# Kernel optimization log

Measured on AMD Instinct MI355X. Metric: run time of the kernel, lower is better.

Reference implementation:

```python
import jax, jax.numpy as jnp
import numpy as np

L, D, H, FF, V = 8, 768, 8, 2048, 32000
MAXLEN, TMAX = 512, 4
S = MAXLEN * TMAX  # 2048 context length
HD = D // H
EPS = 1e-4  # layer_norm_eps from module defaults


def setup_inputs() -> dict:
    key = jax.random.key(0)
    ks = jax.random.split(key, 16)
    s = 0.02
    B = 1
    rn = lambda k, shape: jax.random.normal(k, shape, jnp.float32) * s
    # sinusoidal positional encoding over MAXLEN real-token positions
    pos = np.arange(MAXLEN)[:, None]
    div = np.exp(np.arange(0, D, 2) * (-np.log(10000.0) / D))
    pe = np.zeros((MAXLEN, D), np.float32)
    pe[:, 0::2] = np.sin(pos * div)
    pe[:, 1::2] = np.cos(pos * div)
    return {
        "state_embeddings": jax.random.normal(ks[0], (B, S, D), jnp.float32),
        "padding_mask": jnp.zeros((B, S), bool),
        "pe": jnp.asarray(pe),
        "thought_emb": rn(ks[1], (TMAX, D)),
        "w_qkv": rn(ks[2], (L, 3 * D, D)),
        "b_qkv": jnp.zeros((L, 3 * D), jnp.float32),
        "w_out": rn(ks[3], (L, D, D)),
        "b_out": jnp.zeros((L, D), jnp.float32),
        "ln1_g": jnp.ones((L, D), jnp.float32),
        "ln1_b": jnp.zeros((L, D), jnp.float32),
        "ln2_g": jnp.ones((L, D), jnp.float32),
        "ln2_b": jnp.zeros((L, D), jnp.float32),
        "w_ff1": rn(ks[4], (L, FF, D)),
        "b_ff1": jnp.zeros((L, FF), jnp.float32),
        "w_ff2": rn(ks[5], (L, D, FF)),
        "b_ff2": jnp.zeros((L, D), jnp.float32),
        "fn_g": jnp.ones((D,), jnp.float32),
        "fn_b": jnp.zeros((D,), jnp.float32),
        "w_policy": rn(ks[6], (V, D)),
        "w_v1": rn(ks[7], (FF, D)),
        "b_v1": jnp.zeros((FF,), jnp.float32),
        "w_v2": rn(ks[8], (1, FF)),
        "b_v2": jnp.zeros((1,), jnp.float32),
        "n_thoughts_taken": 3,
    }


def _layer_norm(x, g, b):
    m = x.mean(-1, keepdims=True)
    v = ((x - m) ** 2).mean(-1, keepdims=True)
    return (x - m) / jnp.sqrt(v + EPS) * g + b


def reference(state_embeddings, padding_mask, pe, thought_emb, w_qkv, b_qkv, w_out, b_out, ln1_g, ln1_b, ln2_g, ln2_b, w_ff1, b_ff1, w_ff2, b_ff2, fn_g, fn_b, w_policy, w_v1, b_v1, w_v2, b_v2, n_thoughts_taken):
    tt = int(n_thoughts_taken)
    T = tt + 1  # block size (token + thoughts taken)
    B = state_embeddings.shape[0]
    R = MAXLEN  # real_token_count: all token slots real (no padding)
    # --- DualPositionalEncoding ---
    x = state_embeddings[:, :MAXLEN * T].reshape(B, MAXLEN, T, D)
    x = x + pe[None, :, None, :] + thought_emb[None, None, :T, :]
    x = x.reshape(B, MAXLEN * T, D)
    x = jnp.pad(x, ((0, 0), (0, S - MAXLEN * T), (0, 0)))
    # --- ThoughtsFormer block-causal mask (keep=True means attend) ---
    i = jnp.arange(S)
    tok, off = i // T, i % T
    same_block = (tok[:, None] == tok[None, :]) & (off[:, None] >= off[None, :]) & (tok[:, None] < R)
    global_cols = (off[None, :] == 0) & (tok[None, :] < R) & (i[:, None] > i[None, :]) & (i[:, None] < R * T)
    keep = (same_block | global_cols)[None, None] & (~padding_mask)[:, None, None, :]
    scale = 1.0 / np.sqrt(HD)

    def layer(h, p):
        wq, bq, wo, bo, g1, b1, g2, b2, wf1, bf1, wf2, bf2 = p
        # pre-norm self-attention
        y = _layer_norm(h, g1, b1)
        q, k, v = jnp.split(y @ wq.T + bq, 3, axis=-1)
        q = q.reshape(B, S, H, HD)
        k = k.reshape(B, S, H, HD)
        v = v.reshape(B, S, H, HD)
        scores = jnp.einsum('bihd,bjhd->bhij', q, k) * scale
        attn = jax.nn.softmax(jnp.where(keep, scores, -jnp.inf), axis=-1)
        o = jnp.einsum('bhij,bjhd->bihd', attn, v).reshape(B, S, D)
        h = h + o @ wo.T + bo
        # pre-norm FFN with exact (erf) GELU
        y = _layer_norm(h, g2, b2)
        h = h + jax.nn.gelu(y @ wf1.T + bf1, approximate=False) @ wf2.T + bf2
        h = jnp.where(jnp.isnan(h), 0.0, h)
        return h, None

    x, _ = jax.lax.scan(layer, x, (w_qkv, b_qkv, w_out, b_out, ln1_g, ln1_b, ln2_g, ln2_b, w_ff1, b_ff1, w_ff2, b_ff2))
    x = _layer_norm(x, fn_g, fn_b)  # TransformerEncoder final norm
    logits = x @ w_policy.T  # policy head (no bias)
    values = jax.nn.gelu(x @ w_v1.T + b_v1, approximate=False) @ w_v2.T + b_v2
    return logits, values
```

## Files before the change

kernel.cpp:

```cpp
#include <hip/hip_runtime.h>
#include <math.h>

#define S_TOT 2048
#define DMODEL 768
#define QKVD 2304
#define NHEAD 8
#define HDIM 96
#define FFDIM 2048
#define VOCAB 32000
#define MAXLEN_C 512
#define POL_CHUNK 3200
#define VLT_LD 2080
#define NEG_BIG (-3.0e38f)
#define M_INIT (-1.0e30f)
#define QK_SCALE 0.10206207261596575f

typedef __bf16 bf16x8 __attribute__((ext_vector_type(8)));
typedef float f32x4 __attribute__((ext_vector_type(4)));
typedef unsigned short u16x8 __attribute__((ext_vector_type(8)));
typedef unsigned short u16x4 __attribute__((ext_vector_type(4)));

__device__ __forceinline__ float gelu_exact(float x) {
  return 0.5f * x * (1.0f + erff(x * 0.70710678118654752f));
}

__device__ __forceinline__ float bf2f(unsigned short u) {
  union { unsigned int i; float f; } v;
  v.i = ((unsigned int)u) << 16;
  return v.f;
}

__device__ __forceinline__ unsigned short f2bf(float f) {
  union { float f; unsigned int i; } v;
  v.f = f;
  unsigned int x = v.i;
  return (unsigned short)((x + 0x7fffu + ((x >> 16) & 1u)) >> 16);
}

__device__ __forceinline__ unsigned int pack2bf(float a, float b) {
  return (unsigned int)f2bf(a) | ((unsigned int)f2bf(b) << 16);
}

__device__ __forceinline__ void gload_lds16(const unsigned short* g, unsigned short* l) {
  __builtin_amdgcn_global_load_lds(
      (const __attribute__((address_space(1))) unsigned int*)g,
      (__attribute__((address_space(3))) unsigned int*)l, 16, 0, 0);
}

__global__ __launch_bounds__(256) void embed_kernel(
    const float* __restrict__ se, const float* __restrict__ pe,
    const float* __restrict__ th, const int* __restrict__ ntt,
    float* __restrict__ X) {
  int idx = blockIdx.x * 256 + threadIdx.x;
  if (idx >= S_TOT * DMODEL) return;
  int p = idx / DMODEL;
  int d = idx - p * DMODEL;
  int T = ntt[0] + 1;
  float v = 0.0f;
  if (p < MAXLEN_C * T) {
    v = se[idx] + pe[(p / T) * DMODEL + d] + th[(p % T) * DMODEL + d];
  }
  X[idx] = v;
}

__global__ __launch_bounds__(256) void ln_bf_kernel(
    const float* __restrict__ X, const float* __restrict__ g,
    const float* __restrict__ b, unsigned short* __restrict__ Y) {
  __shared__ float red[4];
  const int row = blockIdx.x;
  const int tid = threadIdx.x;
  const float* x = X + (size_t)row * DMODEL;
  float v0 = x[tid], v1 = x[tid + 256], v2 = x[tid + 512];
  float s = v0 + v1 + v2;
  for (int o = 32; o; o >>= 1) s += __shfl_xor(s, o);
  if ((tid & 63) == 0) red[tid >> 6] = s;
  __syncthreads();
  float mean = (red[0] + red[1] + red[2] + red[3]) * (1.0f / DMODEL);
  float d0 = v0 - mean, d1 = v1 - mean, d2 = v2 - mean;
  float s2 = d0 * d0 + d1 * d1 + d2 * d2;
  for (int o = 32; o; o >>= 1) s2 += __shfl_xor(s2, o);
  __syncthreads();
  if ((tid & 63) == 0) red[tid >> 6] = s2;
  __syncthreads();
  float var = (red[0] + red[1] + red[2] + red[3]) * (1.0f / DMODEL);
  float rstd = rsqrtf(var + 1e-4f);
  unsigned short* y = Y + (size_t)row * DMODEL;
  y[tid]       = f2bf(d0 * rstd * g[tid]       + b[tid]);
  y[tid + 256] = f2bf(d1 * rstd * g[tid + 256] + b[tid + 256]);
  y[tid + 512] = f2bf(d2 * rstd * g[tid + 512] + b[tid + 512]);
}

__global__ __launch_bounds__(256) void cvt_kernel(
    const float* __restrict__ s, unsigned short* __restrict__ d, int n) {
  int i = (blockIdx.x * 256 + threadIdx.x) * 4;
  if (i >= n) return;
  float4 v = *(const float4*)(s + i);
  u16x4 o;
  o[0] = f2bf(v.x); o[1] = f2bf(v.y); o[2] = f2bf(v.z); o[3] = f2bf(v.w);
  *(u16x4*)(d + i) = o;
}

__global__ __launch_bounds__(256) void cvt4_kernel(
    const float* __restrict__ s0, const float* __restrict__ s1,
    const float* __restrict__ s2, const float* __restrict__ s3,
    unsigned short* __restrict__ d0, unsigned short* __restrict__ d1,
    unsigned short* __restrict__ d2, unsigned short* __restrict__ d3,
    int n0, int n1, int n2, int n3) {
  int i = (blockIdx.x * 256 + threadIdx.x) * 4;
  const float* s;
  unsigned short* d;
  if (i < n0) { s = s0; d = d0; }
  else if (i < n0 + n1) { i -= n0; s = s1; d = d1; }
  else if (i < n0 + n1 + n2) { i -= n0 + n1; s = s2; d = d2; }
  else if (i < n0 + n1 + n2 + n3) { i -= n0 + n1 + n2; s = s3; d = d3; }
  else return;
  float4 v = *(const float4*)(s + i);
  u16x4 o;
  o[0] = f2bf(v.x); o[1] = f2bf(v.y); o[2] = f2bf(v.z); o[3] = f2bf(v.w);
  *(u16x4*)(d + i) = o;
}

__global__ __launch_bounds__(256) void cvt6_kernel(
    const float* __restrict__ s0, const float* __restrict__ s1,
    const float* __restrict__ s2, const float* __restrict__ s3,
    const float* __restrict__ s4, const float* __restrict__ s5,
    unsigned short* __restrict__ d0, unsigned short* __restrict__ d1,
    unsigned short* __restrict__ d2, unsigned short* __restrict__ d3,
    unsigned short* __restrict__ d4, unsigned short* __restrict__ d5,
    int n0, int n1, int n2, int n3, int n4, int n5) {
  int i = (blockIdx.x * 256 + threadIdx.x) * 4;
  const float* s;
  unsigned short* d;
  if (i < n0) { s = s0; d = d0; }
  else if (i < n0 + n1) { i -= n0; s = s1; d = d1; }
  else if (i < n0 + n1 + n2) { i -= n0 + n1; s = s2; d = d2; }
  else if (i < n0 + n1 + n2 + n3) { i -= n0 + n1 + n2; s = s3; d = d3; }
  else if (i < n0 + n1 + n2 + n3 + n4) { i -= n0 + n1 + n2 + n3; s = s4; d = d4; }
  else if (i < n0 + n1 + n2 + n3 + n4 + n5) { i -= n0 + n1 + n2 + n3 + n4; s = s5; d = d5; }
  else return;
  float4 v = *(const float4*)(s + i);
  u16x4 o;
  o[0] = f2bf(v.x); o[1] = f2bf(v.y); o[2] = f2bf(v.z); o[3] = f2bf(v.w);
  *(u16x4*)(d + i) = o;
}

__global__ __launch_bounds__(256) void gemm_bf16_kernel(
    const unsigned short* __restrict__ A, const unsigned short* __restrict__ B,
    const float* __restrict__ bias, const float* __restrict__ res,
    void* __restrict__ Cout, int M, int N, int K, int ldc, int act, int outbf,
    int swiz) {
  __shared__ __align__(16) unsigned short As[128 * 32];
  __shared__ __align__(16) unsigned short Bs[128 * 32];
  const int t = threadIdx.x;
  const int w = t >> 6, l = t & 63;
  int n_blk, m_blk;
  if (swiz) {
    const int g = blockIdx.x;
    const int chunk = gridDim.x >> 3;
    const int logical = (g & 7) * chunk + (g >> 3);
    m_blk = logical & 15;
    n_blk = logical >> 4;
  } else {
    n_blk = blockIdx.x; m_blk = blockIdx.y;
  }
  const int n0 = n_blk * 128, i0 = m_blk * 128;
  const int wr = w >> 1, wc = w & 1;
  const int lr = l & 15;
  const int koff = (l >> 4) * 8;

  f32x4 acc[4][4] = {};

  const int srow = t >> 2;
  const int scol = (t & 3) * 8;
  const unsigned short* Ag = A + (size_t)(i0 + srow) * K + scol;
  const unsigned short* Bg = B + (size_t)(n0 + srow) * K + scol;
  unsigned short* Alds0 = &As[(w << 9)];
  unsigned short* Alds1 = &As[2048 + (w << 9)];
  unsigned short* Blds0 = &Bs[(w << 9)];
  unsigned short* Blds1 = &Bs[2048 + (w << 9)];

  for (int k0 = 0; k0 < K; k0 += 32) {
    __syncthreads();
    gload_lds16(Ag + k0, Alds0);
    gload_lds16(Ag + (size_t)64 * K + k0, Alds1);
    gload_lds16(Bg + k0, Blds0);
    gload_lds16(Bg + (size_t)64 * K + k0, Blds1);
    __syncthreads();

    bf16x8 af[4], bfr[4];
#pragma unroll
    for (int fi = 0; fi < 4; ++fi)
      af[fi] = *(const bf16x8*)&As[(wr * 64 + fi * 16 + lr) * 32 + koff];
#pragma unroll
    for (int fj = 0; fj < 4; ++fj)
      bfr[fj] = *(const bf16x8*)&Bs[(wc * 64 + fj * 16 + lr) * 32 + koff];
#pragma unroll
    for (int fi = 0; fi < 4; ++fi)
#pragma unroll
      for (int fj = 0; fj < 4; ++fj)
        acc[fi][fj] = __builtin_amdgcn_mfma_f32_16x16x32_bf16(
            bfr[fj], af[fi], acc[fi][fj], 0, 0, 0);
  }

  const int mloc = l & 15, ng = (l >> 4) * 4;
#pragma unroll
  for (int fi = 0; fi < 4; ++fi) {
    const int i = i0 + wr * 64 + fi * 16 + mloc;
    const size_t rowbase = (size_t)i * ldc;
#pragma unroll
    for (int fj = 0; fj < 4; ++fj) {
      const int nb = n0 + wc * 64 + fj * 16 + ng;
      float z0 = acc[fi][fj][0], z1 = acc[fi][fj][1];
      float z2 = acc[fi][fj][2], z3 = acc[fi][fj][3];
      if (bias) {
        float4 bv = *(const float4*)(bias + nb);
        z0 += bv.x; z1 += bv.y; z2 += bv.z; z3 += bv.w;
      }
      if (act) {
        z0 = gelu_exact(z0); z1 = gelu_exact(z1);
        z2 = gelu_exact(z2); z3 = gelu_exact(z3);
      }
      if (res) {
        float4 rv = *(const float4*)(res + rowbase + nb);
        z0 += rv.x; z1 += rv.y; z2 += rv.z; z3 += rv.w;
      }
      if (outbf) {
        u16x4 o;
        o[0] = f2bf(z0); o[1] = f2bf(z1); o[2] = f2bf(z2); o[3] = f2bf(z3);
        *(u16x4*)((unsigned short*)Cout + rowbase + nb) = o;
      } else {
        *(float4*)((float*)Cout + rowbase + nb) = make_float4(z0, z1, z2, z3);
      }
    }
  }
}

__global__ __launch_bounds__(256) void gemm64_bf16_kernel(
    const unsigned short* __restrict__ A, const unsigned short* __restrict__ B,
    const float* __restrict__ bias, const float* __restrict__ res,
    void* __restrict__ Cout, int M, int N, int K, int ldc, int act, int outbf) {
  __shared__ __align__(16) unsigned short As[2 * 64 * 32];
  __shared__ __align__(16) unsigned short Bs[2 * 64 * 32];
  const int t = threadIdx.x;
  const int w = t >> 6, l = t & 63;
  const int n0 = blockIdx.x * 64, i0 = blockIdx.y * 64;
  const int wr = w >> 1, wc = w & 1;
  const int lr = l & 15;
  const int koff = (l >> 4) * 8;

  f32x4 acc[2][2] = {};

  const int srow = t >> 2;
  const int scol = (t & 3) * 8;
  const unsigned short* Ag = A + (size_t)(i0 + srow) * K + scol;
  const unsigned short* Bg = B + (size_t)(n0 + srow) * K + scol;
  unsigned short* Alds0 = &As[(w << 9)];
  unsigned short* Alds1 = &As[2048 + (w << 9)];
  unsigned short* Blds0 = &Bs[(w << 9)];
  unsigned short* Blds1 = &Bs[2048 + (w << 9)];

  for (int k0 = 0; k0 < K; k0 += 64) {
    __syncthreads();
    gload_lds16(Ag + k0, Alds0);
    gload_lds16(Ag + k0 + 32, Alds1);
    gload_lds16(Bg + k0, Blds0);
    gload_lds16(Bg + k0 + 32, Blds1);
    __syncthreads();

    bf16x8 af[2][2], bfr[2][2];
#pragma unroll
    for (int fi = 0; fi < 2; ++fi)
#pragma unroll
      for (int kk = 0; kk < 2; ++kk)
        af[fi][kk] = *(const bf16x8*)&As[kk * 2048 + (wr * 32 + fi * 16 + lr) * 32 + koff];
#pragma unroll
    for (int fj = 0; fj < 2; ++fj)
#pragma unroll
      for (int kk = 0; kk < 2; ++kk)
        bfr[fj][kk] = *(const bf16x8*)&Bs[kk * 2048 + (wc * 32 + fj * 16 + lr) * 32 + koff];
#pragma unroll
    for (int fi = 0; fi < 2; ++fi)
#pragma unroll
      for (int fj = 0; fj < 2; ++fj)
#pragma unroll
        for (int kk = 0; kk < 2; ++kk)
          acc[fi][fj] = __builtin_amdgcn_mfma_f32_16x16x32_bf16(
              bfr[fj][kk], af[fi][kk], acc[fi][fj], 0, 0, 0);
  }

  const int mloc = l & 15, ng = (l >> 4) * 4;
#pragma unroll
  for (int fi = 0; fi < 2; ++fi) {
    const int i = i0 + wr * 32 + fi * 16 + mloc;
    const size_t rowbase = (size_t)i * ldc;
#pragma unroll
    for (int fj = 0; fj < 2; ++fj) {
      const int nb = n0 + wc * 32 + fj * 16 + ng;
      float z0 = acc[fi][fj][0], z1 = acc[fi][fj][1];
      float z2 = acc[fi][fj][2], z3 = acc[fi][fj][3];
      if (bias) {
        float4 bv = *(const float4*)(bias + nb);
        z0 += bv.x; z1 += bv.y; z2 += bv.z; z3 += bv.w;
      }
      if (act) {
        z0 = gelu_exact(z0); z1 = gelu_exact(z1);
        z2 = gelu_exact(z2); z3 = gelu_exact(z3);
      }
      if (res) {
        float4 rv = *(const float4*)(res + rowbase + nb);
        z0 += rv.x; z1 += rv.y; z2 += rv.z; z3 += rv.w;
      }
      if (outbf) {
        u16x4 o;
        o[0] = f2bf(z0); o[1] = f2bf(z1); o[2] = f2bf(z2); o[3] = f2bf(z3);
        *(u16x4*)((unsigned short*)Cout + rowbase + nb) = o;
      } else {
        *(float4*)((float*)Cout + rowbase + nb) = make_float4(z0, z1, z2, z3);
      }
    }
  }
}

__global__ __launch_bounds__(256) void repack_kernel(
    const unsigned short* __restrict__ qkv, const int* __restrict__ ntt,
    unsigned short* __restrict__ Kg, unsigned short* __restrict__ Vgt,
    unsigned short* __restrict__ Vlt) {
  __shared__ unsigned short vt[64][104];
  const int pb = blockIdx.x * 64, h = blockIdx.y;
  const int T = ntt[0] + 1;
  const int tid = threadIdx.x;

  for (int idx = tid; idx < 64 * 96; idx += 256) {
    int pp = idx / 96, d = idx - pp * 96;
    vt[pp][d] = qkv[(size_t)(pb + pp) * QKVD + 2 * DMODEL + h * HDIM + d];
  }
  const int firstpp = (T - pb % T) % T;
  const int ng = (64 - firstpp + T - 1) / T;
  for (int idx = tid; idx < ng * 96; idx += 256) {
    int gi = idx / 96, d = idx - gi * 96;
    int p = pb + firstpp + gi * T;
    int g = p / T;
    if (g < MAXLEN_C)
      Kg[((size_t)h * 512 + g) * 96 + d] = qkv[(size_t)p * QKVD + DMODEL + h * HDIM + d];
  }
  __syncthreads();
  for (int idx = tid; idx < 96 * 64; idx += 256) {
    int d = idx >> 6, pp = idx & 63;
    Vlt[((size_t)h * 96 + d) * VLT_LD + pb + pp] = vt[pp][d];
  }
  for (int idx = tid; idx < ng * 96; idx += 256) {
    int d = idx / ng, gi = idx - d * ng;
    int pp = firstpp + gi * T;
    int g = (pb + pp) / T;
    if (g < MAXLEN_C && d < 96)
      Vgt[((size_t)h * 96 + d) * 512 + g] = vt[pp][d];
  }
}

__global__ __launch_bounds__(256) void attn_flash_kernel(
    const unsigned short* __restrict__ qkv, const unsigned short* __restrict__ Kg,
    const unsigned short* __restrict__ Vgt, const unsigned short* __restrict__ Vlt,
    const int* __restrict__ ntt, unsigned short* __restrict__ att) {
  __shared__ float Osh[4][96][17];
  __shared__ float Msh[4][16];
  __shared__ float Lsh[4][16];
  const int s = blockIdx.x, h = blockIdx.y;
  const int T = ntt[0] + 1;
  const int tid = threadIdx.x;
  const int w = tid >> 6, l = tid & 63;
  const int q15 = l & 15, grp = l >> 4;
  const int p0 = s * 16;
  const int p = p0 + q15;
  const int myTok = p / T;

  const unsigned short* qrow = qkv + (size_t)p * QKVD + h * HDIM + grp * 8;
  bf16x8 qf0 = *(const bf16x8*)(qrow);
  bf16x8 qf1 = *(const bf16x8*)(qrow + 32);
  bf16x8 qf2 = *(const bf16x8*)(qrow + 64);

  float m_run = M_INIT, l_run = 0.0f;
  f32x4 oacc[6] = {};

  const int gmax = (p0 + 15) / T;
  const int KP = (gmax >> 5) + 1;
  const unsigned short* KgH = Kg + (size_t)h * 512 * 96;
  const unsigned short* VgH = Vgt + (size_t)h * 96 * 512;

  for (int kp = w; kp < KP; kp += 4) {
    f32x4 s0 = {}, s1 = {};
    const unsigned short* k0r = KgH + (size_t)(kp * 32 + q15) * 96 + grp * 8;
    const unsigned short* k1r = k0r + 16 * 96;
    {
      bf16x8 a0 = *(const bf16x8*)(k0r);
      bf16x8 a1 = *(const bf16x8*)(k1r);
      bf16x8 b0 = *(const bf16x8*)(k0r + 32);
      bf16x8 b1 = *(const bf16x8*)(k1r + 32);
      bf16x8 c0 = *(const bf16x8*)(k0r + 64);
      bf16x8 c1 = *(const bf16x8*)(k1r + 64);
      __builtin_amdgcn_s_setprio(1);
      s0 = __builtin_amdgcn_mfma_f32_16x16x32_bf16(a0, qf0, s0, 0, 0, 0);
      s1 = __builtin_amdgcn_mfma_f32_16x16x32_bf16(a1, qf0, s1, 0, 0, 0);
      s0 = __builtin_amdgcn_mfma_f32_16x16x32_bf16(b0, qf1, s0, 0, 0, 0);
      s1 = __builtin_amdgcn_mfma_f32_16x16x32_bf16(b1, qf1, s1, 0, 0, 0);
      s0 = __builtin_amdgcn_mfma_f32_16x16x32_bf16(c0, qf2, s0, 0, 0, 0);
      s1 = __builtin_amdgcn_mfma_f32_16x16x32_bf16(c1, qf2, s1, 0, 0, 0);
      __builtin_amdgcn_s_setprio(0);
    }
    float sc[8];
#pragma unroll
    for (int e = 0; e < 4; ++e) {
      int g = kp * 32 + grp * 4 + e;
      sc[e] = (g * T <= p) ? s0[e] * QK_SCALE : NEG_BIG;
      g += 16;
      sc[4 + e] = (g * T <= p) ? s1[e] * QK_SCALE : NEG_BIG;
    }
    float tmax = sc[0];
#pragma unroll
    for (int e = 1; e < 8; ++e) tmax = fmaxf(tmax, sc[e]);
    tmax = fmaxf(tmax, __shfl_xor(tmax, 16));
    tmax = fmaxf(tmax, __shfl_xor(tmax, 32));
    float mnew = fmaxf(m_run, tmax);
    float alpha = __expf(m_run - mnew);
    float pv[8], ps = 0.0f;
#pragma unroll
    for (int e = 0; e < 8; ++e) { pv[e] = __expf(sc[e] - mnew); ps += pv[e]; }
    ps += __shfl_xor(ps, 16);
    ps += __shfl_xor(ps, 32);
    l_run = l_run * alpha + ps;
    m_run = mnew;
#pragma unroll
    for (int dt = 0; dt < 6; ++dt) oacc[dt] *= alpha;
    unsigned int pk0[2], pk1[2];
    pk0[0] = pack2bf(pv[0], pv[1]); pk0[1] = pack2bf(pv[2], pv[3]);
    pk1[0] = pack2bf(pv[4], pv[5]); pk1[1] = pack2bf(pv[6], pv[7]);
    union { unsigned int u[4]; bf16x8 v; } pf;
#pragma unroll
    for (int w2 = 0; w2 < 4; ++w2) {
      int src = (((grp & 1) << 1) + (w2 >> 1)) * 16 + q15;
      int y0 = __shfl((int)pk0[w2 & 1], src);
      int y1 = __shfl((int)pk1[w2 & 1], src);
      pf.u[w2] = (grp >> 1) ? (unsigned int)y1 : (unsigned int)y0;
    }
    __builtin_amdgcn_s_setprio(1);
#pragma unroll
    for (int dt = 0; dt < 6; ++dt) {
      bf16x8 vf = *(const bf16x8*)(VgH + (size_t)(dt * 16 + q15) * 512 + kp * 32 + grp * 8);
      oacc[dt] = __builtin_amdgcn_mfma_f32_16x16x32_bf16(vf, pf.v, oacc[dt], 0, 0, 0);
    }
    __builtin_amdgcn_s_setprio(0);
  }

  if (w == 3) {
    f32x4 s0 = {};
    const unsigned short* kl = qkv + (size_t)(p0 + q15) * QKVD + DMODEL + h * HDIM + grp * 8;
    __builtin_amdgcn_s_setprio(1);
    s0 = __builtin_amdgcn_mfma_f32_16x16x32_bf16(*(const bf16x8*)(kl), qf0, s0, 0, 0, 0);
    s0 = __builtin_amdgcn_mfma_f32_16x16x32_bf16(*(const bf16x8*)(kl + 32), qf1, s0, 0, 0, 0);
    s0 = __builtin_amdgcn_mfma_f32_16x16x32_bf16(*(const bf16x8*)(kl + 64), qf2, s0, 0, 0, 0);
    __builtin_amdgcn_s_setprio(0);
    float sc[4];
#pragma unroll
    for (int e = 0; e < 4; ++e) {
      int pk = p0 + grp * 4 + e;
      bool ok = (pk / T == myTok) && (pk % T != 0) && (pk <= p);
      sc[e] = ok ? s0[e] * QK_SCALE : NEG_BIG;
    }
    float tmax = fmaxf(fmaxf(sc[0], sc[1]), fmaxf(sc[2], sc[3]));
    tmax = fmaxf(tmax, __shfl_xor(tmax, 16));
    tmax = fmaxf(tmax, __shfl_xor(tmax, 32));
    float mnew = fmaxf(m_run, tmax);
    float alpha = __expf(m_run - mnew);
    float pv[4], ps = 0.0f;
#pragma unroll
    for (int e = 0; e < 4; ++e) { pv[e] = __expf(sc[e] - mnew); ps += pv[e]; }
    ps += __shfl_xor(ps, 16);
    ps += __shfl_xor(ps, 32);
    l_run = l_run * alpha + ps;
    m_run = mnew;
#pragma unroll
    for (int dt = 0; dt < 6; ++dt) oacc[dt] *= alpha;
    unsigned int pk0[2];
    pk0[0] = pack2bf(pv[0], pv[1]); pk0[1] = pack2bf(pv[2], pv[3]);
    union { unsigned int u[4]; bf16x8 v; } pf;
#pragma unroll
    for (int w2 = 0; w2 < 4; ++w2) {
      int src = (((grp & 1) << 1) + (w2 >> 1)) * 16 + q15;
      int y0 = __shfl((int)pk0[w2 & 1], src);
      pf.u[w2] = (grp >> 1) ? 0u : (unsigned int)y0;
    }
    __builtin_amdgcn_s_setprio(1);
#pragma unroll
    for (int dt = 0; dt < 6; ++dt) {
      bf16x8 vf = *(const bf16x8*)(Vlt + ((size_t)h * 96 + dt * 16 + q15) * VLT_LD + p0 + grp * 8);
      oacc[dt] = __builtin_amdgcn_mfma_f32_16x16x32_bf16(vf, pf.v, oacc[dt], 0, 0, 0);
    }
    __builtin_amdgcn_s_setprio(0);
  }

  if (l < 16) { Msh[w][l] = m_run; Lsh[w][l] = l_run; }
#pragma unroll
  for (int dt = 0; dt < 6; ++dt)
#pragma unroll
    for (int e = 0; e < 4; ++e)
      Osh[w][dt * 16 + grp * 4 + e][q15] = oacc[dt][e];
  __syncthreads();

  {
    const int q = tid & 15, dg = tid >> 4;
    float m0 = Msh[0][q], m1 = Msh[1][q], m2 = Msh[2][q], m3 = Msh[3][q];
    float ms = fmaxf(fmaxf(m0, m1), fmaxf(m2, m3));
    float c0 = __expf(m0 - ms), c1 = __expf(m1 - ms);
    float c2 = __expf(m2 - ms), c3 = __expf(m3 - ms);
    float lsum = c0 * Lsh[0][q] + c1 * Lsh[1][q] + c2 * Lsh[2][q] + c3 * Lsh[3][q];
    float rinv = 1.0f / lsum;
    unsigned short* orow = att + (size_t)(p0 + q) * DMODEL + h * HDIM;
#pragma unroll
    for (int j = 0; j < 6; ++j) {
      int d = dg * 6 + j;
      float o = c0 * Osh[0][d][q] + c1 * Osh[1][d][q] +
                c2 * Osh[2][d][q] + c3 * Osh[3][d][q];
      orow[d] = f2bf(o * rinv);
    }
  }
}

__global__ __launch_bounds__(256) void v2_kernel(
    const unsigned short* __restrict__ F1, const float* __restrict__ w2,
    const float* __restrict__ b2, float* __restrict__ out) {
  __shared__ float red[4];
  const int row = blockIdx.x;
  const int tid = threadIdx.x;
  float s = 0.0f;
  const unsigned short* xr = F1 + (size_t)row * FFDIM;
  for (int f = tid; f < FFDIM; f += 256) s += bf2f(xr[f]) * w2[f];
  for (int o = 32; o; o >>= 1) s += __shfl_xor(s, o);
  if ((tid & 63) == 0) red[tid >> 6] = s;
  __syncthreads();
  if (tid == 0) out[row] = red[0] + red[1] + red[2] + red[3] + b2[0];
}

extern "C" void kernel_launch(void* const* d_in, const int* in_sizes, int n_in,
                              void* d_out, int out_size, void* d_ws, size_t ws_size,
                              hipStream_t stream) {
  const float* se      = (const float*)d_in[0];
  const float* pe      = (const float*)d_in[2];
  const float* th      = (const float*)d_in[3];
  const float* w_qkv   = (const float*)d_in[4];
  const float* b_qkv   = (const float*)d_in[5];
  const float* w_out   = (const float*)d_in[6];
  const float* b_out   = (const float*)d_in[7];
  const float* ln1_g   = (const float*)d_in[8];
  const float* ln1_b   = (const float*)d_in[9];
  const float* ln2_g   = (const float*)d_in[10];
  const float* ln2_b   = (const float*)d_in[11];
  const float* w_ff1   = (const float*)d_in[12];
  const float* b_ff1   = (const float*)d_in[13];
  const float* w_ff2   = (const float*)d_in[14];
  const float* b_ff2   = (const float*)d_in[15];
  const float* fn_g    = (const float*)d_in[16];
  const float* fn_b    = (const float*)d_in[17];
  const float* w_pol   = (const float*)d_in[18];
  const float* w_v1    = (const float*)d_in[19];
  const float* b_v1    = (const float*)d_in[20];
  const float* w_v2    = (const float*)d_in[21];
  const float* b_v2    = (const float*)d_in[22];
  const int*   ntt     = (const int*)d_in[23];

  float* logits = (float*)d_out;
  float* values = logits + (size_t)S_TOT * VOCAB;

  const int nq = 3 * DMODEL * DMODEL, no = DMODEL * DMODEL;
  const int nf1 = FFDIM * DMODEL, nf2 = DMODEL * FFDIM;
  const int npol = VOCAB * DMODEL;

  char* p = (char*)d_ws;
  float* X             = (float*)p;          p += (size_t)S_TOT * DMODEL * 4;
  unsigned short* Ybf  = (unsigned short*)p; p += (size_t)S_TOT * DMODEL * 2;
  unsigned short* QKVb = (unsigned short*)p; p += (size_t)S_TOT * QKVD * 2;
  unsigned short* ATTb = (unsigned short*)p; p += (size_t)S_TOT * DMODEL * 2;
  unsigned short* F1b  = (unsigned short*)p; p += (size_t)S_TOT * FFDIM * 2;
  unsigned short* Kg   = (unsigned short*)p; p += (size_t)NHEAD * 512 * 96 * 2;
  unsigned short* Vgt  = (unsigned short*)p; p += (size_t)NHEAD * 96 * 512 * 2;
  unsigned short* Vlt  = (unsigned short*)p; p += (size_t)NHEAD * 96 * VLT_LD * 2;

  const size_t wbytes = ((size_t)8 * (nq + no + nf1 + nf2) + npol + nf1) * 2;
  const size_t used   = (size_t)(p - (char*)d_ws);
  const bool bigws = ws_size >= used + wbytes + (1u << 20);

  unsigned short *WqA, *WoA, *Wf1A, *Wf2A, *WpolA, *Wv1A;
  if (bigws) {
    WqA   = (unsigned short*)p; p += (size_t)8 * nq * 2;
    WoA   = (unsigned short*)p; p += (size_t)8 * no * 2;
    Wf1A  = (unsigned short*)p; p += (size_t)8 * nf1 * 2;
    Wf2A  = (unsigned short*)p; p += (size_t)8 * nf2 * 2;
    WpolA = (unsigned short*)p; p += (size_t)npol * 2;
    Wv1A  = (unsigned short*)p;
  } else {
    WqA   = (unsigned short*)p; p += (size_t)nq * 2;
    WoA   = (unsigned short*)p; p += (size_t)no * 2;
    Wf1A  = (unsigned short*)p; p += (size_t)nf1 * 2;
    Wf2A  = (unsigned short*)p; p += (size_t)nf2 * 2;
    WpolA = (unsigned short*)p;
    Wv1A  = Wf1A;
  }

  dim3 blk(256);

  if (bigws) {
    const int t0 = 8 * nq, t1 = 8 * no, t2 = 8 * nf1, t3 = 8 * nf2;
    const long total = (long)t0 + t1 + t2 + t3 + npol + nf1;
    cvt6_kernel<<<dim3((unsigned)((total / 4 + 255) / 256)), blk, 0, stream>>>(
        w_qkv, w_out, w_ff1, w_ff2, w_pol, w_v1,
        WqA, WoA, Wf1A, Wf2A, WpolA, Wv1A,
        t0, t1, t2, t3, npol, nf1);
  }

  embed_kernel<<<dim3((S_TOT * DMODEL + 255) / 256), blk, 0, stream>>>(se, pe, th, ntt, X);

  for (int l = 0; l < 8; ++l) {
    const unsigned short* pWq  = bigws ? WqA  + (size_t)l * nq  : WqA;
    const unsigned short* pWo  = bigws ? WoA  + (size_t)l * no  : WoA;
    const unsigned short* pWf1 = bigws ? Wf1A + (size_t)l * nf1 : Wf1A;
    const unsigned short* pWf2 = bigws ? Wf2A + (size_t)l * nf2 : Wf2A;
    if (!bigws) {
      const int ncvt4 = (nq + no + nf1 + nf2) / 4;
      cvt4_kernel<<<dim3((ncvt4 + 255) / 256), blk, 0, stream>>>(
          w_qkv + (size_t)l * nq, w_out + (size_t)l * no,
          w_ff1 + (size_t)l * nf1, w_ff2 + (size_t)l * nf2,
          WqA, WoA, Wf1A, Wf2A, nq, no, nf1, nf2);
    }

    ln_bf_kernel<<<dim3(S_TOT), blk, 0, stream>>>(X, ln1_g + l * DMODEL, ln1_b + l * DMODEL, Ybf);
    gemm_bf16_kernel<<<dim3(QKVD / 128, S_TOT / 128), blk, 0, stream>>>(
        Ybf, pWq, b_qkv + (size_t)l * 3 * DMODEL, nullptr, QKVb,
        S_TOT, QKVD, DMODEL, QKVD, 0, 1, 0);
    repack_kernel<<<dim3(S_TOT / 64, NHEAD), blk, 0, stream>>>(QKVb, ntt, Kg, Vgt, Vlt);
    attn_flash_kernel<<<dim3(S_TOT / 16, NHEAD), blk, 0, stream>>>(
        QKVb, Kg, Vgt, Vlt, ntt, ATTb);
    gemm64_bf16_kernel<<<dim3(DMODEL / 64, S_TOT / 64), blk, 0, stream>>>(
        ATTb, pWo, b_out + (size_t)l * DMODEL, X, X,
        S_TOT, DMODEL, DMODEL, DMODEL, 0, 0);

    ln_bf_kernel<<<dim3(S_TOT), blk, 0, stream>>>(X, ln2_g + l * DMODEL, ln2_b + l * DMODEL, Ybf);
    gemm_bf16_kernel<<<dim3(FFDIM / 128, S_TOT / 128), blk, 0, stream>>>(
        Ybf, pWf1, b_ff1 + (size_t)l * FFDIM, nullptr, F1b,
        S_TOT, FFDIM, DMODEL, FFDIM, 1, 1, 0);
    gemm64_bf16_kernel<<<dim3(DMODEL / 64, S_TOT / 64), blk, 0, stream>>>(
        F1b, pWf2, b_ff2 + (size_t)l * DMODEL, X, X,
        S_TOT, DMODEL, FFDIM, DMODEL, 0, 0);
  }

  ln_bf_kernel<<<dim3(S_TOT), blk, 0, stream>>>(X, fn_g, fn_b, Ybf);

  if (bigws) {
    gemm_bf16_kernel<<<dim3((S_TOT / 128) * (VOCAB / 128)), blk, 0, stream>>>(
        Ybf, WpolA, nullptr, nullptr, logits, S_TOT, VOCAB, DMODEL, VOCAB, 0, 0, 1);
  } else {
    for (int c = 0; c < VOCAB / POL_CHUNK; ++c) {
      cvt_kernel<<<dim3((POL_CHUNK * DMODEL / 4 + 255) / 256), blk, 0, stream>>>(
          w_pol + (size_t)c * POL_CHUNK * DMODEL, WpolA, POL_CHUNK * DMODEL);
      gemm_bf16_kernel<<<dim3(POL_CHUNK / 128, S_TOT / 128), blk, 0, stream>>>(
          Ybf, WpolA, nullptr, nullptr, logits + (size_t)c * POL_CHUNK,
          S_TOT, POL_CHUNK, DMODEL, VOCAB, 0, 0, 0);
    }
  }

  if (!bigws)
    cvt_kernel<<<dim3((nf1 / 4 + 255) / 256), blk, 0, stream>>>(w_v1, Wv1A, nf1);
  gemm_bf16_kernel<<<dim3(FFDIM / 128, S_TOT / 128), blk, 0, stream>>>(
      Ybf, Wv1A, b_v1, nullptr, F1b, S_TOT, FFDIM, DMODEL, FFDIM, 1, 1, 0);
  v2_kernel<<<dim3(S_TOT), blk, 0, stream>>>(F1b, w_v2, b_v2, values);
}
```

Measured before the change: 1.518 ms.

## Double-buffer LDS in bf16 GEMM kernels to overlap global loads with MFMA

Both GEMM kernels switch from a single LDS buffer, loaded and consumed between two barriers, to a ping-pong double buffer. The next k-tile's direct-to-LDS loads are issued before computing on the current one, with an explicit vmcnt wait and raw s_barrier plus sched_barrier fences. The aim is to hide global load latency behind the matrix math. In exchange it doubles LDS use per block, which may lower occupancy, and correctness depends on the hand-tuned vmcnt count matching the four loads issued per stage.

```diff
diff --git a/kernel.cpp b/kernel.cpp
--- a/kernel.cpp
+++ b/kernel.cpp
@@ -149,8 +149,8 @@
     const float* __restrict__ bias, const float* __restrict__ res,
     void* __restrict__ Cout, int M, int N, int K, int ldc, int act, int outbf,
     int swiz) {
-  __shared__ __align__(16) unsigned short As[128 * 32];
-  __shared__ __align__(16) unsigned short Bs[128 * 32];
+  __shared__ __align__(16) unsigned short As[2 * 4096];
+  __shared__ __align__(16) unsigned short Bs[2 * 4096];
   const int t = threadIdx.x;
   const int w = t >> 6, l = t & 63;
   int n_blk, m_blk;
@@ -174,33 +174,49 @@
   const int scol = (t & 3) * 8;
   const unsigned short* Ag = A + (size_t)(i0 + srow) * K + scol;
   const unsigned short* Bg = B + (size_t)(n0 + srow) * K + scol;
-  unsigned short* Alds0 = &As[(w << 9)];
-  unsigned short* Alds1 = &As[2048 + (w << 9)];
-  unsigned short* Blds0 = &Bs[(w << 9)];
-  unsigned short* Blds1 = &Bs[2048 + (w << 9)];
-
-  for (int k0 = 0; k0 < K; k0 += 32) {
-    __syncthreads();
-    gload_lds16(Ag + k0, Alds0);
-    gload_lds16(Ag + (size_t)64 * K + k0, Alds1);
-    gload_lds16(Bg + k0, Blds0);
-    gload_lds16(Bg + (size_t)64 * K + k0, Blds1);
-    __syncthreads();
-
-    bf16x8 af[4], bfr[4];
-#pragma unroll
-    for (int fi = 0; fi < 4; ++fi)
-      af[fi] = *(const bf16x8*)&As[(wr * 64 + fi * 16 + lr) * 32 + koff];
-#pragma unroll
-    for (int fj = 0; fj < 4; ++fj)
-      bfr[fj] = *(const bf16x8*)&Bs[(wc * 64 + fj * 16 + lr) * 32 + koff];
-#pragma unroll
-    for (int fi = 0; fi < 4; ++fi)
-#pragma unroll
-      for (int fj = 0; fj < 4; ++fj)
-        acc[fi][fj] = __builtin_amdgcn_mfma_f32_16x16x32_bf16(
-            bfr[fj], af[fi], acc[fi][fj], 0, 0, 0);
-  }
+  const int lo0 = (w << 9);
+  const int lo1 = 2048 + (w << 9);
+
+#define STAGE128(buf, k0)                                        \
+  do {                                                           \
+    gload_lds16(Ag + (k0), &As[(buf) * 4096 + lo0]);             \
+    gload_lds16(Ag + (size_t)64 * K + (k0), &As[(buf) * 4096 + lo1]); \
+    gload_lds16(Bg + (k0), &Bs[(buf) * 4096 + lo0]);             \
+    gload_lds16(Bg + (size_t)64 * K + (k0), &Bs[(buf) * 4096 + lo1]); \
+  } while (0)
+
+#define COMPUTE128(buf)                                                   \
+  do {                                                                    \
+    const unsigned short* Ab = &As[(buf) * 4096];                         \
+    const unsigned short* Bb = &Bs[(buf) * 4096];                         \
+    bf16x8 af[4], bfr[4];                                                 \
+    _Pragma("unroll") for (int fi = 0; fi < 4; ++fi)                      \
+        af[fi] = *(const bf16x8*)&Ab[(wr * 64 + fi * 16 + lr) * 32 + koff]; \
+    _Pragma("unroll") for (int fj = 0; fj < 4; ++fj)                      \
+        bfr[fj] = *(const bf16x8*)&Bb[(wc * 64 + fj * 16 + lr) * 32 + koff]; \
+    _Pragma("unroll") for (int fi = 0; fi < 4; ++fi)                      \
+      _Pragma("unroll") for (int fj = 0; fj < 4; ++fj)                    \
+          acc[fi][fj] = __builtin_amdgcn_mfma_f32_16x16x32_bf16(          \
+              bfr[fj], af[fi], acc[fi][fj], 0, 0, 0);                     \
+  } while (0)
+
+  const int nt = K >> 5;
+  STAGE128(0, 0);
+  int cur = 0;
+  for (int tt = 0; tt < nt - 1; ++tt) {
+    STAGE128(cur ^ 1, (tt + 1) << 5);
+    asm volatile("s_waitcnt vmcnt(4)" ::: "memory");
+    __builtin_amdgcn_s_barrier();
+    __builtin_amdgcn_sched_barrier(0);
+    COMPUTE128(cur);
+    __builtin_amdgcn_sched_barrier(0);
+    __builtin_amdgcn_s_barrier();
+    cur ^= 1;
+  }
+  asm volatile("s_waitcnt vmcnt(0)" ::: "memory");
+  __builtin_amdgcn_s_barrier();
+  __builtin_amdgcn_sched_barrier(0);
+  COMPUTE128(cur);
 
   const int mloc = l & 15, ng = (l >> 4) * 4;
 #pragma unroll
@@ -233,14 +249,16 @@
       }
     }
   }
+#undef STAGE128
+#undef COMPUTE128
 }
 
 __global__ __launch_bounds__(256) void gemm64_bf16_kernel(
     const unsigned short* __restrict__ A, const unsigned short* __restrict__ B,
     const float* __restrict__ bias, const float* __restrict__ res,
     void* __restrict__ Cout, int M, int N, int K, int ldc, int act, int outbf) {
-  __shared__ __align__(16) unsigned short As[2 * 64 * 32];
-  __shared__ __align__(16) unsigned short Bs[2 * 64 * 32];
+  __shared__ __align__(16) unsigned short As[2 * 4096];
+  __shared__ __align__(16) unsigned short Bs[2 * 4096];
   const int t = threadIdx.x;
   const int w = t >> 6, l = t & 63;
   const int n0 = blockIdx.x * 64, i0 = blockIdx.y * 64;
@@ -254,39 +272,52 @@
   const int scol = (t & 3) * 8;
   const unsigned short* Ag = A + (size_t)(i0 + srow) * K + scol;
   const unsigned short* Bg = B + (size_t)(n0 + srow) * K + scol;
-  unsigned short* Alds0 = &As[(w << 9)];
-  unsigned short* Alds1 = &As[2048 + (w << 9)];
-  unsigned short* Blds0 = &Bs[(w << 9)];
-  unsigned short* Blds1 = &Bs[2048 + (w << 9)];
-
-  for (int k0 = 0; k0 < K; k0 += 64) {
-    __syncthreads();
-    gload_lds16(Ag + k0, Alds0);
-    gload_lds16(Ag + k0 + 32, Alds1);
-    gload_lds16(Bg + k0, Blds0);
-    gload_lds16(Bg + k0 + 32, Blds1);
-    __syncthreads();
-
-    bf16x8 af[2][2], bfr[2][2];
-#pragma unroll
-    for (int fi = 0; fi < 2; ++fi)
-#pragma unroll
-      for (int kk = 0; kk < 2; ++kk)
-        af[fi][kk] = *(const bf16x8*)&As[kk * 2048 + (wr * 32 + fi * 16 + lr) * 32 + koff];
-#pragma unroll
-    for (int fj = 0; fj < 2; ++fj)
-#pragma unroll
-      for (int kk = 0; kk < 2; ++kk)
-        bfr[fj][kk] = *(const bf16x8*)&Bs[kk * 2048 + (wc * 32 + fj * 16 + lr) * 32 + koff];
-#pragma unroll
-    for (int fi = 0; fi < 2; ++fi)
-#pragma unroll
-      for (int fj = 0; fj < 2; ++fj)
-#pragma unroll
-        for (int kk = 0; kk < 2; ++kk)
-          acc[fi][fj] = __builtin_amdgcn_mfma_f32_16x16x32_bf16(
-              bfr[fj][kk], af[fi][kk], acc[fi][fj], 0, 0, 0);
-  }
+  const int lo0 = (w << 9);
+  const int lo1 = 2048 + (w << 9);
+
+#define STAGE64(buf, k0)                                      \
+  do {                                                        \
+    gload_lds16(Ag + (k0), &As[(buf) * 4096 + lo0]);          \
+    gload_lds16(Ag + (k0) + 32, &As[(buf) * 4096 + lo1]);     \
+    gload_lds16(Bg + (k0), &Bs[(buf) * 4096 + lo0]);          \
+    gload_lds16(Bg + (k0) + 32, &Bs[(buf) * 4096 + lo1]);     \
+  } while (0)
+
+#define COMPUTE64(buf)                                                        \
+  do {                                                                        \
+    const unsigned short* Ab = &As[(buf) * 4096];                             \
+    const unsigned short* Bb = &Bs[(buf) * 4096];                             \
+    bf16x8 af[2][2], bfr[2][2];                                               \
+    _Pragma("unroll") for (int fi = 0; fi < 2; ++fi)                          \
+      _Pragma("unroll") for (int kk = 0; kk < 2; ++kk)                        \
+          af[fi][kk] = *(const bf16x8*)&Ab[kk * 2048 + (wr * 32 + fi * 16 + lr) * 32 + koff]; \
+    _Pragma("unroll") for (int fj = 0; fj < 2; ++fj)                          \
+      _Pragma("unroll") for (int kk = 0; kk < 2; ++kk)                        \
+          bfr[fj][kk] = *(const bf16x8*)&Bb[kk * 2048 + (wc * 32 + fj * 16 + lr) * 32 + koff]; \
+    _Pragma("unroll") for (int fi = 0; fi < 2; ++fi)                          \
+      _Pragma("unroll") for (int fj = 0; fj < 2; ++fj)                        \
+        _Pragma("unroll") for (int kk = 0; kk < 2; ++kk)                      \
+            acc[fi][fj] = __builtin_amdgcn_mfma_f32_16x16x32_bf16(            \
+                bfr[fj][kk], af[fi][kk], acc[fi][fj], 0, 0, 0);               \
+  } while (0)
+
+  const int nt = K >> 6;
+  STAGE64(0, 0);
+  int cur = 0;
+  for (int tt = 0; tt < nt - 1; ++tt) {
+    STAGE64(cur ^ 1, (tt + 1) << 6);
+    asm volatile("s_waitcnt vmcnt(4)" ::: "memory");
+    __builtin_amdgcn_s_barrier();
+    __builtin_amdgcn_sched_barrier(0);
+    COMPUTE64(cur);
+    __builtin_amdgcn_sched_barrier(0);
+    __builtin_amdgcn_s_barrier();
+    cur ^= 1;
+  }
+  asm volatile("s_waitcnt vmcnt(0)" ::: "memory");
+  __builtin_amdgcn_s_barrier();
+  __builtin_amdgcn_sched_barrier(0);
+  COMPUTE64(cur);
 
   const int mloc = l & 15, ng = (l >> 4) * 4;
 #pragma unroll
@@ -319,6 +350,8 @@
       }
     }
   }
+#undef STAGE64
+#undef COMPUTE64
 }
 
 __global__ __launch_bounds__(256) void repack_kernel(
```

New measurement: 1.439 ms. 1.05x faster.
